# Optimization experiments

Hardware: AMD Instinct MI355X
Metric: run time of the kernel (lower is better)

## Reference

```python
import jax, jax.numpy as jnp
import numpy as np

H, W = 160, 160
FS = 7
SPAN = FS // 2
NUM_CLASSES = 19
NUM_ITERS = 5
THETA_ALPHA = 160.0  # scales rgb in bilateral features
THETA_BETA = 3.0     # scales position in bilateral features
THETA_GAMMA = 3.0    # scales position in spatial features
EPS = 1e-20

# offsets ordered (dx outer, dy inner) to match TF filter-tap index (dx+span)*FS + (dy+span)
OFFSETS = [(dx, dy) for dx in range(-SPAN, SPAN + 1) for dy in range(-SPAN, SPAN + 1)]


def _make_filter(features):
    # features: (bs, cf, H, W) -> gaussian affinity filter (bs, FS*FS, H, W)
    # filter[b, k, i, j] = exp(-0.5 * ||f[b,:,i+dx,j+dy] - f[b,:,i,j]||^2), 0 if out of bounds
    fp = jnp.pad(features, ((0, 0), (0, 0), (SPAN, SPAN), (SPAN, SPAN)))
    rows = jnp.arange(H)
    cols = jnp.arange(W)
    taps = []
    for dx, dy in OFFSETS:
        shifted = fp[:, :, SPAN + dx:SPAN + dx + H, SPAN + dy:SPAN + dy + W]
        aff = jnp.exp(-0.5 * jnp.sum((features - shifted) ** 2, axis=1))  # (bs, H, W)
        mask = (((rows + dx >= 0) & (rows + dx < H))[:, None]
                & ((cols + dy >= 0) & (cols + dy < W))[None, :])
        taps.append(aff * mask)
    return jnp.stack(taps, axis=1)  # (bs, FS*FS, H, W)


def _patches(x):
    # x: (bs, C, H, W) -> (bs, C, FS*FS, H, W), zero-padded shifts (matches extract_patches SAME)
    xp = jnp.pad(x, ((0, 0), (0, 0), (SPAN, SPAN), (SPAN, SPAN)))
    return jnp.stack(
        [xp[:, :, SPAN + dx:SPAN + dx + H, SPAN + dy:SPAN + dy + W] for dx, dy in OFFSETS],
        axis=2)


def _compute_gaussian(x, filt):
    # x: (bs, C, H, W), filt: (bs, FS*FS, H, W) -> (bs, C, H, W)
    return jnp.sum(_patches(x) * filt[:, None], axis=2)


def _forward(unaries, rgb, spatial_ker_weights, bilateral_ker_weights, compatibility_matrix):
    u = jnp.transpose(unaries, (0, 3, 1, 2))     # (bs, C, H, W)
    rgb_nchw = jnp.transpose(rgb, (0, 3, 1, 2))  # (bs, 3, H, W)
    bs = u.shape[0]
    mesh = jnp.stack(
        jnp.meshgrid(jnp.arange(H, dtype=jnp.float32), jnp.arange(W, dtype=jnp.float32),
                     indexing='ij'), 0)          # (2, H, W)
    spatial_feat = jnp.broadcast_to((mesh / THETA_GAMMA)[None], (bs, 2, H, W))
    bilateral_feat = jnp.concatenate(
        [rgb_nchw / THETA_ALPHA,
         jnp.broadcast_to((mesh / THETA_BETA)[None], (bs, 2, H, W))], axis=1)  # (bs, 5, H, W)

    spatial_filter = _make_filter(spatial_feat)
    bilateral_filter = _make_filter(bilateral_feat)

    ones = jnp.ones_like(u)
    spatial_norm = _compute_gaussian(ones, spatial_filter)
    bilateral_norm = _compute_gaussian(ones, bilateral_filter)

    q = u
    for _ in range(NUM_ITERS):
        # NOTE: original code does tf.nn.softmax(q_values, 0) -> softmax over the BATCH axis.
        sm = jax.nn.softmax(q, axis=0)
        s_out = _compute_gaussian(sm, spatial_filter) / (spatial_norm + EPS)
        b_out = _compute_gaussian(sm, bilateral_filter) / (bilateral_norm + EPS)
        msg = (jnp.einsum('kc,bchw->bkhw', spatial_ker_weights, s_out)
               + jnp.einsum('kc,bchw->bkhw', bilateral_ker_weights, b_out))
        pairwise = jnp.einsum('kc,bchw->bkhw', compatibility_matrix, msg)
        q = u - pairwise
    return jnp.transpose(q, (0, 2, 3, 1))  # (bs, H, W, C)


def setup_inputs() -> dict:
    key = jax.random.key(0)
    k1, k2 = jax.random.split(key)
    unaries = jax.random.normal(k1, (2, H, W, NUM_CLASSES), dtype=jnp.float32)
    rgb = jax.random.uniform(k2, (2, H, W, 3), dtype=jnp.float32) * 255.0
    eye = jnp.eye(NUM_CLASSES, dtype=jnp.float32)
    return {
        'unaries': unaries,
        'rgb': rgb,
        'spatial_ker_weights': eye,            # _diagonal_initializer
        'bilateral_ker_weights': eye,          # _diagonal_initializer
        'compatibility_matrix': -eye,          # _potts_model_initializer
    }


def reference(unaries, rgb, spatial_ker_weights, bilateral_ker_weights, compatibility_matrix):
    return _forward(unaries, rgb, spatial_ker_weights, bilateral_ker_weights,
                    compatibility_matrix)
```

## Files before the change

### kernel.cpp

```cpp
#include <hip/hip_runtime.h>


typedef __attribute__((ext_vector_type(4))) _Float16 half4;
typedef __attribute__((ext_vector_type(2))) _Float16 half2f;
typedef __attribute__((ext_vector_type(4))) float float4v;

#define HH 160
#define WW 160
#define NPIX (HH*WW)
#define NC 19
#define NG 5
#define SPAN 3
#define TR 8
#define TC 16
#define NPXT 128
#define LR 14
#define LC 22
#define LCP 24
#define HSTRIDE (LR*LCP)
#define NHALO (LR*LC)
#define NRING 180
#define NBLK 200
#define NTHR 640
#define EPSF 1e-20f
#define MAGICV 0x5EEDF00Du

#define EPW(b) (32 + (b)*32)

#define SZ_A    30720
#define OFF_WB  SZ_A
#define SHM_SZ  (SZ_A + 25*128*8)

__device__ __forceinline__ float fast_rcp(float x) { return __builtin_amdgcn_rcpf(x); }

__device__ __forceinline__ float smx0(float q0, float q1) {
    const float m  = fmaxf(q0, q1);
    const float e0 = __expf(q0 - m);
    const float e1 = __expf(q1 - m);
    return e0 * fast_rcp(e0 + e1);
}

__global__ void __launch_bounds__(NTHR) crf_kernel(
        const float* __restrict__ u,
        const float* __restrict__ rgb,
        const float* __restrict__ sw,
        const float* __restrict__ bw,
        const float* __restrict__ compat,
        unsigned long long* __restrict__ gsmA,
        unsigned long long* __restrict__ gsmB,
        unsigned* __restrict__ bar,
        float* __restrict__ out) {
    __shared__ __align__(16) char shm[SHM_SZ];
    __shared__ float Msh[960];
    __shared__ float rowsum[NC];
    __shared__ int   diagflag;
    float4*   rgbL = (float4*)shm;
    half4*    smH  = (half4*)shm;
    float*    accF = (float*)shm;
    unsigned* wbW  = (unsigned*)(shm + OFF_WB);
    const uint2* wbP = (const uint2*)(shm + OFF_WB);

    constexpr float WSPC[49] = {
        0.36787944f,0.48567179f,0.57375342f,0.60653066f,0.57375342f,0.48567179f,0.36787944f,
        0.48567179f,0.64118039f,0.75746513f,0.80073740f,0.75746513f,0.64118039f,0.48567179f,
        0.57375342f,0.75746513f,0.89483932f,0.94595947f,0.89483932f,0.75746513f,0.57375342f,
        0.60653066f,0.80073740f,0.94595947f,1.00000000f,0.94595947f,0.80073740f,0.60653066f,
        0.57375342f,0.75746513f,0.89483932f,0.94595947f,0.89483932f,0.75746513f,0.57375342f,
        0.48567179f,0.64118039f,0.75746513f,0.80073740f,0.75746513f,0.64118039f,0.48567179f,
        0.36787944f,0.48567179f,0.57375342f,0.60653066f,0.57375342f,0.48567179f,0.36787944f };

    const int tid = threadIdx.x;
    const int px  = tid & 127;
    const int g   = tid >> 7;
    const int r   = px >> 4, c = px & 15;
    const int ti0 = blockIdx.y * TR, tj0 = blockIdx.x * TC;
    const int gp  = (ti0 + r) * WW + (tj0 + c);
    const int ctr = (r + SPAN) * LCP + (c + SPAN);
    const int ku  = 4 * g;
    const int bid = blockIdx.y * 10 + blockIdx.x;

    int nb[8];
    {
        const int bx = blockIdx.x, by = blockIdx.y;
        int k = 0;
        #pragma unroll
        for (int dy2 = -1; dy2 <= 1; ++dy2)
            #pragma unroll
            for (int dx2 = -1; dx2 <= 1; ++dx2) {
                if (dx2 == 0 && dy2 == 0) continue;
                const int nx = bx + dx2, ny = by + dy2;
                nb[k++] = ((unsigned)nx < 10u && (unsigned)ny < 20u) ? (ny*10 + nx) : bid;
            }
    }

    if (bid == 0) {
        for (int e = tid; e < NBLK; e += NTHR)
            __hip_atomic_store(&bar[EPW(e)], 0u, __ATOMIC_RELAXED, __HIP_MEMORY_SCOPE_AGENT);
        __syncthreads();
        if (tid == 0)
            __hip_atomic_store(&bar[0], MAGICV, __ATOMIC_RELEASE, __HIP_MEMORY_SCOPE_AGENT);
    }
    if (tid == 0) {
        diagflag = 1;
        while (__hip_atomic_load(&bar[0], __ATOMIC_ACQUIRE, __HIP_MEMORY_SCOPE_AGENT) != MAGICV)
            __builtin_amdgcn_s_sleep(2);
    }
    if (tid < NC) {
        float rs = 0.0f;
        for (int cb = 0; cb < NC; ++cb) rs += sw[tid*NC + cb] + bw[tid*NC + cb];
        rowsum[tid] = rs;
    }
    __syncthreads();

    for (int e = tid; e < 960; e += NTHR) {
        const int k = e / 48, cc2 = e % 48;
        float acc = 0.0f;
        if (k < NC) {
            if (cc2 < NC) {
                for (int j = 0; j < NC; ++j) acc += compat[k*NC + j] * sw[j*NC + cc2];
            } else if (cc2 >= 20 && cc2 < 20 + NC) {
                const int cb = cc2 - 20;
                for (int j = 0; j < NC; ++j) acc += compat[k*NC + j] * bw[j*NC + cb];
            } else if (cc2 == 40) {
                for (int j = 0; j < NC; ++j) acc += compat[k*NC + j] * rowsum[j];
            }
        }
        Msh[e] = acc;
        bool off = false;
        if (k < NC) {
            if (cc2 < NC && cc2 != k && acc != 0.0f) off = true;
            if (cc2 >= 20 && cc2 < 20 + NC && (cc2 - 20) != k && acc != 0.0f) off = true;
        }
        if (off) atomicAnd(&diagflag, 0);
    }
    __syncthreads();

    float dsv[4], dbv[4];
    #pragma unroll
    for (int i = 0; i < 4; ++i) {
        dsv[i] = Msh[(ku + i) * 48 + (ku + i)];
        dbv[i] = Msh[(ku + i) * 48 + 20 + (ku + i)];
    }
    const bool isdiag = (diagflag != 0);

    for (int e = tid; e < 2 * NHALO; e += NTHR) {
        const int bb = e / NHALO, pos = e % NHALO;
        const int hr = pos / LC, hc = pos % LC;
        const int yi = ti0 - SPAN + hr, xj = tj0 - SPAN + hc;
        float4 rv = make_float4(0.f, 0.f, 0.f, 0.f);
        if ((unsigned)yi < HH && (unsigned)xj < WW) {
            const float* p = rgb + ((size_t)(bb * NPIX) + yi * WW + xj) * 3;
            rv = make_float4(p[0]*(1.f/160.f), p[1]*(1.f/160.f), p[2]*(1.f/160.f), 1.f);
        }
        rgbL[(bb ? HSTRIDE : 0) + hr * LCP + hc] = rv;
    }
    __syncthreads();

    {
        const float4 cv0 = rgbL[ctr];
        const float4 cv1 = rgbL[HSTRIDE + ctr];
        const int tapb = g * 10;
        const int ntap = (g == 4) ? 9 : 10;
        for (int i = 0; i < ntap; ++i) {
            const int t = tapb + i;
            const int dx = t / 7 - SPAN, dy = t % 7 - SPAN;
            const int n = ctr + dx * LCP + dy;
            const float4 nv0 = rgbL[n];
            const float4 nv1 = rgbL[HSTRIDE + n];
            const float wsm = __expf(-(float)(dx*dx + dy*dy) * (1.f/18.f)) * nv0.w;
            const float dr0 = cv0.x-nv0.x, dg0 = cv0.y-nv0.y, db0 = cv0.z-nv0.z;
            const float dr1 = cv1.x-nv1.x, dg1 = cv1.y-nv1.y, db1 = cv1.z-nv1.z;
            const float wb0 = wsm * __expf(-0.5f*(dr0*dr0+dg0*dg0+db0*db0));
            const float wb1 = wsm * __expf(-0.5f*(dr1*dr1+dg1*dg1+db1*db1));
            half2f hw = {(_Float16)wb0, (_Float16)wb1};
            unsigned uw; __builtin_memcpy(&uw, &hw, 4);
            wbW[(t >> 1) * 256 + px * 2 + (t & 1)] = uw;
        }
        if (g == 4) wbW[24 * 256 + px * 2 + 1] = 0u;
    }
    __syncthreads();

    float snI, bnI0, bnI1;
    {
        float sn = 0.f, bn0 = 0.f, bn1 = 0.f;
        #pragma unroll
        for (int t = 0; t < 49; ++t) {
            const unsigned uw = wbW[(t >> 1) * 256 + px * 2 + (t & 1)];
            half2f hw; __builtin_memcpy(&hw, &uw, 4);
            bn0 += (float)hw.x; bn1 += (float)hw.y;
            const int dx = t / 7 - SPAN, dy = t % 7 - SPAN;
            const int yi = ti0 + r + dx, xj = tj0 + c + dy;
            sn += (((unsigned)yi < HH) && ((unsigned)xj < WW)) ? WSPC[t] : 0.0f;
        }
        snI  = fast_rcp(sn + EPSF);
        bnI0 = fast_rcp(bn0 + EPSF);
        bnI1 = fast_rcp(bn1 + EPSF);
    }

    float uv0[4], uv1[4];
    #pragma unroll
    for (int i = 0; i < 4; ++i) {
        const int ch = 4*g + i;
        uv0[i] = (ch < NC) ? u[(size_t)gp * NC + ch] : 0.0f;
        uv1[i] = (ch < NC) ? u[((size_t)NPIX + gp) * NC + ch] : 0.0f;
    }
    half4 sh;
    #pragma unroll
    for (int i = 0; i < 4; ++i) sh[i] = (_Float16)smx0(uv0[i], uv1[i]);

    for (int it = 0; it < 5; ++it) {
        {
            unsigned long long u64; __builtin_memcpy(&u64, &sh, 8);
            unsigned long long* gdst = ((it & 1) ? gsmB : gsmA);
            __hip_atomic_store(&gdst[g * NPIX + gp], u64,
                               __ATOMIC_RELAXED, __HIP_MEMORY_SCOPE_AGENT);
        }
        __syncthreads();
        if (tid == 0) {
            __hip_atomic_store(&bar[EPW(bid)], (unsigned)(it + 1),
                               __ATOMIC_RELAXED, __HIP_MEMORY_SCOPE_AGENT);
            const unsigned tgt = (unsigned)(it + 1);
            unsigned mn;
            do {
                mn = 0xFFFFFFFFu;
                #pragma unroll
                for (int k = 0; k < 8; ++k) {
                    const unsigned e = __hip_atomic_load(&bar[EPW(nb[k])],
                                                         __ATOMIC_RELAXED, __HIP_MEMORY_SCOPE_AGENT);
                    mn = (e < mn) ? e : mn;
                }
                if (mn < tgt) __builtin_amdgcn_s_sleep(1);
            } while (mn < tgt);
        }
        __syncthreads();

        const unsigned long long* gsrc = ((it & 1) ? gsmB : gsmA);
        smH[g * HSTRIDE + ctr] = sh;
        #pragma unroll
        for (int k2 = 0; k2 < 2; ++k2) {
            const int e = tid + NTHR * k2;
            if (e < NG * NRING) {
                const int sg = e / NRING, re = e - sg * NRING;
                int hr, hc;
                if (re < 66)        { hr = re / 22;          hc = re % 22; }
                else if (re < 132)  { const int t2 = re - 66;  hr = 11 + t2 / 22; hc = t2 % 22; }
                else                { const int t2 = re - 132; hr = 3 + t2 / 6;
                                      const int s = t2 % 6;    hc = (s < 3) ? s : s + 16; }
                const int yi = ti0 - SPAN + hr, xj = tj0 - SPAN + hc;
                half4 hv = (half4)(_Float16)0.0f;
                if ((unsigned)yi < HH && (unsigned)xj < WW) {
                    const unsigned long long raw =
                        __hip_atomic_load(&gsrc[sg * NPIX + yi * WW + xj],
                                          __ATOMIC_RELAXED, __HIP_MEMORY_SCOPE_AGENT);
                    __builtin_memcpy(&hv, &raw, 8);
                }
                smH[sg * HSTRIDE + hr * LCP + hc] = hv;
            }
        }
        __syncthreads();

        float4v sAv = (float4v)0.0f, b0a = (float4v)0.0f, b1a = (float4v)0.0f;
        const half4* pl = smH + g * HSTRIDE;
        #pragma unroll
        for (int i = 0; i < 24; ++i) {
            const uint2 wp = wbP[i * 128 + px];
            #pragma unroll
            for (int s = 0; s < 2; ++s) {
                const int t = 2*i + s;
                const int dx = t / 7 - SPAN, dy = t % 7 - SPAN;
                half2f hw; __builtin_memcpy(&hw, s ? &wp.y : &wp.x, 4);
                const float w0 = (float)hw.x, w1 = (float)hw.y;
                const half4 v = pl[ctr + dx*LCP + dy];
                const float4v f = {(float)v[0], (float)v[1], (float)v[2], (float)v[3]};
                sAv += WSPC[t] * f;
                b0a += w0 * f;
                b1a += w1 * f;
            }
        }
        {
            const uint2 wp = wbP[24 * 128 + px];
            half2f hw; __builtin_memcpy(&hw, &wp.x, 4);
            const float w0 = (float)hw.x, w1 = (float)hw.y;
            const half4 v = pl[ctr + SPAN*LCP + SPAN];
            const float4v f = {(float)v[0], (float)v[1], (float)v[2], (float)v[3]};
            sAv += WSPC[48] * f;
            b0a += w0 * f;
            b1a += w1 * f;
        }

        float q0v[4], q1v[4];
        if (isdiag) {
            #pragma unroll
            for (int i = 0; i < 4; ++i) {
                const float sAn = sAv[i] * snI;
                const float b0n = b0a[i] * bnI0;
                const float b1x = b1a[i] * bnI1;
                q0v[i] = uv0[i] - dsv[i]*sAn - dbv[i]*b0n;
                q1v[i] = uv1[i] - (dsv[i] + dbv[i]) + dsv[i]*sAn + dbv[i]*b1x;
            }
        } else {
            __syncthreads();
            #pragma unroll
            for (int i = 0; i < 4; ++i) {
                accF[(4*g + i) * NPXT + px]      = sAv[i] * snI;
                accF[(20 + 4*g + i) * NPXT + px] = b0a[i] * bnI0;
                accF[(40 + 4*g + i) * NPXT + px] = b1a[i] * bnI1;
            }
            __syncthreads();
            float t1[4] = {0,0,0,0}, t2[4] = {0,0,0,0}, t3[4] = {0,0,0,0};
            #pragma unroll
            for (int cc = 0; cc < 20; ++cc) {
                const float sv  = accF[cc * NPXT + px];
                const float b0v = accF[(20 + cc) * NPXT + px];
                const float b1v = accF[(40 + cc) * NPXT + px];
                #pragma unroll
                for (int i = 0; i < 4; ++i) {
                    const float* mk = Msh + (ku + i) * 48;
                    t1[i] += mk[cc] * sv;
                    t2[i] += mk[20 + cc] * b0v;
                    t3[i] += mk[20 + cc] * b1v;
                }
            }
            #pragma unroll
            for (int i = 0; i < 4; ++i) {
                const float rs = Msh[(ku + i) * 48 + 40];
                q0v[i] = uv0[i] - t1[i] - t2[i];
                q1v[i] = uv1[i] - rs + t1[i] + t3[i];
            }
        }

        if (it == 4) {
            #pragma unroll
            for (int i = 0; i < 4; ++i) {
                const int ch = 4*g + i;
                if (ch < NC) {
                    out[(size_t)gp * NC + ch]          = q0v[i];
                    out[((size_t)NPIX + gp) * NC + ch] = q1v[i];
                }
            }
        } else {
            #pragma unroll
            for (int i = 0; i < 4; ++i) sh[i] = (_Float16)smx0(q0v[i], q1v[i]);
        }
    }
}

extern "C" void kernel_launch(void* const* d_in, const int* in_sizes, int n_in,
                              void* d_out, int out_size, void* d_ws, size_t ws_size,
                              hipStream_t stream) {
    const float* u      = (const float*)d_in[0];
    const float* rgb    = (const float*)d_in[1];
    const float* sw     = (const float*)d_in[2];
    const float* bw     = (const float*)d_in[3];
    const float* compat = (const float*)d_in[4];
    float* out = (float*)d_out;

    unsigned long long* gsmA = (unsigned long long*)d_ws;
    unsigned long long* gsmB = (unsigned long long*)((char*)d_ws + 1024000);
    unsigned* bar = (unsigned*)((char*)d_ws + 2048000);

    crf_kernel<<<dim3(WW/TC, HH/TR, 1), dim3(NTHR), 0, stream>>>(
        u, rgb, sw, bw, compat, gsmA, gsmB, bar, out);
}
```

Before: 107.9 us.

## Drop global init barrier, use tagged epoch flags and fp32 LDS halo

Removes the grid-wide startup barrier where block 0 zeroed the flags, and replaces it with tagged epoch words so blocks can start immediately. The initial softmax publish and each later iteration's publish move earlier, overlapping with setup and compute. The shared-memory halo is stored as fp32 with a padded stride, which removes half-to-float conversions in the 49-tap inner loop and reduces bank conflicts. The risk is that flags from a previous launch still carry the tag and a high epoch, which could let a block pass its wait before neighbours have written.

```diff
diff --git a/kernel.cpp b/kernel.cpp
--- a/kernel.cpp
+++ b/kernel.cpp
@@ -18,12 +18,16 @@
 #define LC 22
 #define LCP 24
 #define HSTRIDE (LR*LCP)
+#define LCP_F 25
+#define HS_F (LR*LCP_F)
 #define NHALO (LR*LC)
 #define NRING 180
 #define NBLK 200
 #define NTHR 640
 #define EPSF 1e-20f
-#define MAGICV 0x5EEDF00Du
+
+#define EPTAG   0x5EED0000u
+#define EPMASK  0xFFFF0000u
 
 #define EPW(b) (32 + (b)*32)
 
@@ -38,6 +42,10 @@
     const float e0 = __expf(q0 - m);
     const float e1 = __expf(q1 - m);
     return e0 * fast_rcp(e0 + e1);
+}
+
+__device__ __forceinline__ unsigned ep_decode(unsigned w) {
+    return ((w & EPMASK) == EPTAG) ? (w & 0xFFFFu) : 0u;
 }
 
 __global__ void __launch_bounds__(NTHR) crf_kernel(
@@ -55,7 +63,7 @@
     __shared__ float rowsum[NC];
     __shared__ int   diagflag;
     float4*   rgbL = (float4*)shm;
-    half4*    smH  = (half4*)shm;
+    float4v*  smF  = (float4v*)shm;
     float*    accF = (float*)shm;
     unsigned* wbW  = (unsigned*)(shm + OFF_WB);
     const uint2* wbP = (const uint2*)(shm + OFF_WB);
@@ -75,7 +83,8 @@
     const int r   = px >> 4, c = px & 15;
     const int ti0 = blockIdx.y * TR, tj0 = blockIdx.x * TC;
     const int gp  = (ti0 + r) * WW + (tj0 + c);
-    const int ctr = (r + SPAN) * LCP + (c + SPAN);
+    const int ctr  = (r + SPAN) * LCP   + (c + SPAN);
+    const int ctrF = (r + SPAN) * LCP_F + (c + SPAN);
     const int ku  = 4 * g;
     const int bid = blockIdx.y * 10 + blockIdx.x;
 
@@ -93,24 +102,37 @@
             }
     }
 
-    if (bid == 0) {
-        for (int e = tid; e < NBLK; e += NTHR)
-            __hip_atomic_store(&bar[EPW(e)], 0u, __ATOMIC_RELAXED, __HIP_MEMORY_SCOPE_AGENT);
-        __syncthreads();
-        if (tid == 0)
-            __hip_atomic_store(&bar[0], MAGICV, __ATOMIC_RELEASE, __HIP_MEMORY_SCOPE_AGENT);
-    }
-    if (tid == 0) {
-        diagflag = 1;
-        while (__hip_atomic_load(&bar[0], __ATOMIC_ACQUIRE, __HIP_MEMORY_SCOPE_AGENT) != MAGICV)
-            __builtin_amdgcn_s_sleep(2);
-    }
+    if (tid == 0) diagflag = 1;
+
+    float uv0[4], uv1[4];
+    #pragma unroll
+    for (int i = 0; i < 4; ++i) {
+        const int ch = 4*g + i;
+        uv0[i] = (ch < NC) ? u[(size_t)gp * NC + ch] : 0.0f;
+        uv1[i] = (ch < NC) ? u[((size_t)NPIX + gp) * NC + ch] : 0.0f;
+    }
+    half4 sh;
+    float smv[4];
+    #pragma unroll
+    for (int i = 0; i < 4; ++i) {
+        smv[i] = smx0(uv0[i], uv1[i]);
+        sh[i]  = (_Float16)smv[i];
+    }
+    {
+        unsigned long long u64; __builtin_memcpy(&u64, &sh, 8);
+        __hip_atomic_store(&gsmA[g * NPIX + gp], u64,
+                           __ATOMIC_RELAXED, __HIP_MEMORY_SCOPE_AGENT);
+    }
+
     if (tid < NC) {
         float rs = 0.0f;
         for (int cb = 0; cb < NC; ++cb) rs += sw[tid*NC + cb] + bw[tid*NC + cb];
         rowsum[tid] = rs;
     }
     __syncthreads();
+    if (tid == 0)
+        __hip_atomic_store(&bar[EPW(bid)], EPTAG | 1u,
+                           __ATOMIC_RELAXED, __HIP_MEMORY_SCOPE_AGENT);
 
     for (int e = tid; e < 960; e += NTHR) {
         const int k = e / 48, cc2 = e % 48;
@@ -197,45 +219,35 @@
         bnI1 = fast_rcp(bn1 + EPSF);
     }
 
-    float uv0[4], uv1[4];
-    #pragma unroll
-    for (int i = 0; i < 4; ++i) {
-        const int ch = 4*g + i;
-        uv0[i] = (ch < NC) ? u[(size_t)gp * NC + ch] : 0.0f;
-        uv1[i] = (ch < NC) ? u[((size_t)NPIX + gp) * NC + ch] : 0.0f;
-    }
-    half4 sh;
-    #pragma unroll
-    for (int i = 0; i < 4; ++i) sh[i] = (_Float16)smx0(uv0[i], uv1[i]);
-
     for (int it = 0; it < 5; ++it) {
+        __syncthreads();
+
         {
-            unsigned long long u64; __builtin_memcpy(&u64, &sh, 8);
-            unsigned long long* gdst = ((it & 1) ? gsmB : gsmA);
-            __hip_atomic_store(&gdst[g * NPIX + gp], u64,
-                               __ATOMIC_RELAXED, __HIP_MEMORY_SCOPE_AGENT);
-        }
-        __syncthreads();
+            const float4v sv = {smv[0], smv[1], smv[2], smv[3]};
+            smF[g * HS_F + ctrF] = sv;
+        }
+
         if (tid == 0) {
-            __hip_atomic_store(&bar[EPW(bid)], (unsigned)(it + 1),
-                               __ATOMIC_RELAXED, __HIP_MEMORY_SCOPE_AGENT);
-            const unsigned tgt = (unsigned)(it + 1);
+            const unsigned seq = (unsigned)(it + 1);
+            if (it > 0)
+                __hip_atomic_store(&bar[EPW(bid)], EPTAG | seq,
+                                   __ATOMIC_RELAXED, __HIP_MEMORY_SCOPE_AGENT);
             unsigned mn;
             do {
-                mn = 0xFFFFFFFFu;
+                mn = 0xFFFFu;
                 #pragma unroll
                 for (int k = 0; k < 8; ++k) {
-                    const unsigned e = __hip_atomic_load(&bar[EPW(nb[k])],
+                    const unsigned w = __hip_atomic_load(&bar[EPW(nb[k])],
                                                          __ATOMIC_RELAXED, __HIP_MEMORY_SCOPE_AGENT);
+                    const unsigned e = ep_decode(w);
                     mn = (e < mn) ? e : mn;
                 }
-                if (mn < tgt) __builtin_amdgcn_s_sleep(1);
-            } while (mn < tgt);
+                if (mn < seq) __builtin_amdgcn_s_sleep(1);
+            } while (mn < seq);
         }
         __syncthreads();
 
         const unsigned long long* gsrc = ((it & 1) ? gsmB : gsmA);
-        smH[g * HSTRIDE + ctr] = sh;
         #pragma unroll
         for (int k2 = 0; k2 < 2; ++k2) {
             const int e = tid + NTHR * k2;
@@ -247,20 +259,21 @@
                 else                { const int t2 = re - 132; hr = 3 + t2 / 6;
                                       const int s = t2 % 6;    hc = (s < 3) ? s : s + 16; }
                 const int yi = ti0 - SPAN + hr, xj = tj0 - SPAN + hc;
-                half4 hv = (half4)(_Float16)0.0f;
+                float4v fv = (float4v)0.0f;
                 if ((unsigned)yi < HH && (unsigned)xj < WW) {
                     const unsigned long long raw =
                         __hip_atomic_load(&gsrc[sg * NPIX + yi * WW + xj],
                                           __ATOMIC_RELAXED, __HIP_MEMORY_SCOPE_AGENT);
-                    __builtin_memcpy(&hv, &raw, 8);
+                    half4 hv; __builtin_memcpy(&hv, &raw, 8);
+                    fv = (float4v){(float)hv[0], (float)hv[1], (float)hv[2], (float)hv[3]};
                 }
-                smH[sg * HSTRIDE + hr * LCP + hc] = hv;
+                smF[sg * HS_F + hr * LCP_F + hc] = fv;
             }
         }
         __syncthreads();
 
         float4v sAv = (float4v)0.0f, b0a = (float4v)0.0f, b1a = (float4v)0.0f;
-        const half4* pl = smH + g * HSTRIDE;
+        const float4v* pl = smF + g * HS_F;
         #pragma unroll
         for (int i = 0; i < 24; ++i) {
             const uint2 wp = wbP[i * 128 + px];
@@ -270,8 +283,7 @@
                 const int dx = t / 7 - SPAN, dy = t % 7 - SPAN;
                 half2f hw; __builtin_memcpy(&hw, s ? &wp.y : &wp.x, 4);
                 const float w0 = (float)hw.x, w1 = (float)hw.y;
-                const half4 v = pl[ctr + dx*LCP + dy];
-                const float4v f = {(float)v[0], (float)v[1], (float)v[2], (float)v[3]};
+                const float4v f = pl[ctrF + dx*LCP_F + dy];
                 sAv += WSPC[t] * f;
                 b0a += w0 * f;
                 b1a += w1 * f;
@@ -281,8 +293,7 @@
             const uint2 wp = wbP[24 * 128 + px];
             half2f hw; __builtin_memcpy(&hw, &wp.x, 4);
             const float w0 = (float)hw.x, w1 = (float)hw.y;
-            const half4 v = pl[ctr + SPAN*LCP + SPAN];
-            const float4v f = {(float)v[0], (float)v[1], (float)v[2], (float)v[3]};
+            const float4v f = pl[ctrF + SPAN*LCP_F + SPAN];
             sAv += WSPC[48] * f;
             b0a += w0 * f;
             b1a += w1 * f;
@@ -340,7 +351,14 @@
             }
         } else {
             #pragma unroll
-            for (int i = 0; i < 4; ++i) sh[i] = (_Float16)smx0(q0v[i], q1v[i]);
+            for (int i = 0; i < 4; ++i) {
+                smv[i] = smx0(q0v[i], q1v[i]);
+                sh[i]  = (_Float16)smv[i];
+            }
+            unsigned long long u64; __builtin_memcpy(&u64, &sh, 8);
+            unsigned long long* gdst = (((it + 1) & 1) ? gsmB : gsmA);
+            __hip_atomic_store(&gdst[g * NPIX + gp], u64,
+                               __ATOMIC_RELAXED, __HIP_MEMORY_SCOPE_AGENT);
         }
     }
 }
```

Measured after the change: 103.1 us. 1.05x faster.
